# Performance work log

Measured on AMD Instinct MI355X. Metric: run time of the kernel, lower is better.

Reference implementation:

```python
import jax, jax.numpy as jnp
import numpy as np

B, C, HH, WW = 8, 640, 32, 32
NH = 8            # num heads
GROUPS = 32       # GroupNorm groups (normalization(channels))
EPS = 1e-5


def group_norm(x, w, b):
    # x: [B, C, H, W]; GroupNorm over (C/G, H, W) per group
    bb, c, hh, ww = x.shape
    xg = x.reshape(bb, GROUPS, c // GROUPS, hh, ww)
    mu = xg.mean(axis=(2, 3, 4), keepdims=True)
    var = xg.var(axis=(2, 3, 4), keepdims=True)
    xg = (xg - mu) * jax.lax.rsqrt(var + EPS)
    x = xg.reshape(bb, c, hh, ww)
    return x * w[None, :, None, None] + b[None, :, None, None]


def setup_inputs() -> dict:
    key = jax.random.key(0)
    ks = jax.random.split(key, 4)
    x = jax.random.normal(ks[0], (B, C, HH, WW), dtype=jnp.float32)
    norm_w = jnp.ones((C,), dtype=jnp.float32)
    norm_b = jnp.zeros((C,), dtype=jnp.float32)
    # 1x1 conv weights (squeezed to [out, in]); scaled for numerical sanity.
    qkv_w = jax.random.normal(ks[1], (3 * C, C), dtype=jnp.float32) / np.sqrt(C)
    qkv_b = jnp.zeros((3 * C,), dtype=jnp.float32)
    # proj_out is zero_module in the original; use random weights so the math is exercised.
    proj_w = jax.random.normal(ks[2], (C, C), dtype=jnp.float32) / np.sqrt(C)
    proj_b = jnp.zeros((C,), dtype=jnp.float32)
    return {"x": x, "norm_w": norm_w, "norm_b": norm_b,
            "qkv_w": qkv_w, "qkv_b": qkv_b, "proj_w": proj_w, "proj_b": proj_b}


def reference(x, norm_w, norm_b, qkv_w, qkv_b, proj_w, proj_b):
    b, c, hh, ww = x.shape
    T = hh * ww
    d = c // NH  # head dim
    xn = group_norm(x, norm_w, norm_b).reshape(b, c, T)          # [B,C,T]
    qkv = jnp.einsum('oc,bct->bot', qkv_w, xn) + qkv_b[None, :, None]  # [B,3C,T]
    # legacy layout: width = (three, heads, d)
    qkv = qkv.reshape(b, 3, NH, d, T)
    q, k, v = qkv[:, 0], qkv[:, 1], qkv[:, 2]                    # each [B,H,D,T]
    scale = 1.0 / jnp.sqrt(jnp.sqrt(jnp.float32(d)))
    scores = jnp.einsum('bhdt,bhds->bhts', q * scale, k * scale)  # [B,H,T,T]
    w = jax.nn.softmax(scores, axis=-1)
    a = jnp.einsum('bhts,bhds->bhdt', w, v).reshape(b, c, T)     # [B,C,T]
    h = jnp.einsum('oc,bct->bot', proj_w, a) + proj_b[None, :, None]
    return x + h.reshape(b, c, hh, ww)
```

## Files before the change

kernel.cpp:

```cpp
#include <hip/hip_runtime.h>

#define B_   8
#define C_   640
#define T_   1024
#define NH_  8
#define D_   80
#define DP_  96

typedef __attribute__((ext_vector_type(8))) short s16x8;
typedef __attribute__((ext_vector_type(4))) float f32x4;

__device__ __forceinline__ unsigned short f2b(float f) {
  unsigned u = __builtin_bit_cast(unsigned, f);
  u += 0x7FFFu + ((u >> 16) & 1u);
  return (unsigned short)(u >> 16);
}
__device__ __forceinline__ unsigned short f2bt(float f) {
  return (unsigned short)(__builtin_bit_cast(unsigned, f) >> 16);
}

__device__ __forceinline__ void gl_lds(const unsigned short* gp, unsigned short* lp) {
  __builtin_amdgcn_global_load_lds(
      (const __attribute__((address_space(1))) unsigned int*)gp,
      (__attribute__((address_space(3))) unsigned int*)lp, 16, 0, 0);
}

__global__ __launch_bounds__(256) void pre_kernel(
    const float* __restrict__ x, const float* __restrict__ w,
    const float* __restrict__ bias, unsigned short* __restrict__ xnt,
    const float* __restrict__ qw, const float* __restrict__ pw,
    unsigned short* __restrict__ oq, unsigned short* __restrict__ op) {
  const int tid = threadIdx.x;
  if (blockIdx.x >= 256) {
    const int NQ = 3 * C_ * C_ / 4, NP = C_ * C_ / 4;
    int i = (blockIdx.x - 256) * 256 + tid;
    for (; i < NQ + NP; i += 400 * 256) {
      const bool q = i < NQ;
      const float4 v = q ? ((const float4*)qw)[i] : ((const float4*)pw)[i - NQ];
      ushort4 o;
      o.x = f2b(v.x); o.y = f2b(v.y); o.z = f2b(v.z); o.w = f2b(v.w);
      if (q) ((ushort4*)oq)[i] = o; else ((ushort4*)op)[i - NQ] = o;
    }
    return;
  }
  const int b = blockIdx.x >> 5, g = blockIdx.x & 31;
  const size_t base = ((size_t)b * C_ + g * 20) * T_;
  float s = 0.f, ss = 0.f;
  for (int i = tid; i < 20 * T_; i += 256) {
    const float v = x[base + i];
    s += v; ss += v * v;
  }
  #pragma unroll
  for (int mask = 1; mask < 64; mask <<= 1) {
    s += __shfl_xor(s, mask); ss += __shfl_xor(ss, mask);
  }
  __shared__ float red[2][4];
  if ((tid & 63) == 0) { red[0][tid >> 6] = s; red[1][tid >> 6] = ss; }
  __syncthreads();
  s  = red[0][0] + red[0][1] + red[0][2] + red[0][3];
  ss = red[1][0] + red[1][1] + red[1][2] + red[1][3];
  const float mu   = s * (1.f / 20480.f);
  const float var  = ss * (1.f / 20480.f) - mu * mu;
  const float rstd = rsqrtf(var + 1e-5f);
  float ac[20], bc[20];
  #pragma unroll
  for (int c = 0; c < 20; c++) {
    const float wc = w[g * 20 + c];
    ac[c] = wc * rstd;
    bc[c] = bias[g * 20 + c] - mu * ac[c];
  }
  for (int tc = tid; tc < T_; tc += 256) {
    const size_t xoff = base + tc;
    unsigned short* dst = xnt + ((size_t)b * T_ + tc) * C_ + g * 20;
    #pragma unroll
    for (int j = 0; j < 5; j++) {
      ushort4 o;
      o.x = f2b(x[xoff + (size_t)(j * 4 + 0) * T_] * ac[j * 4 + 0] + bc[j * 4 + 0]);
      o.y = f2b(x[xoff + (size_t)(j * 4 + 1) * T_] * ac[j * 4 + 1] + bc[j * 4 + 1]);
      o.z = f2b(x[xoff + (size_t)(j * 4 + 2) * T_] * ac[j * 4 + 2] + bc[j * 4 + 2]);
      o.w = f2b(x[xoff + (size_t)(j * 4 + 3) * T_] * ac[j * 4 + 3] + bc[j * 4 + 3]);
      *(ushort4*)(dst + j * 4) = o;
    }
  }
}

template <int MODE>
__global__ __launch_bounds__(MODE == 0 ? 512 : 256, 4) void gemm_mfma(
    const unsigned short* __restrict__ Wb, const unsigned short* __restrict__ Xb,
    const float* __restrict__ bias, const float* __restrict__ resid,
    unsigned short* __restrict__ qg, unsigned short* __restrict__ kg,
    unsigned short* __restrict__ vg, float* __restrict__ outf) {
  constexpr int AUSH = MODE == 0 ? 4096 : 2048;
  constexpr int BUFU = MODE == 0 ? 12288 : 6144;
  constexpr int MF   = MODE == 0 ? 4 : 2;
  constexpr int NIT  = C_ / 32;
  __shared__ __align__(16) char smem[MODE == 0 ? 73728 : 36864];
  unsigned short* const sm = (unsigned short*)smem;
  const int tid = threadIdx.x;
  const int lane = tid & 63, wvi = tid >> 6;
  const int wm = MODE == 0 ? (wvi >> 2) : (wvi >> 1);
  const int wn = MODE == 0 ? (wvi & 3) : (wvi & 1);
  const int rl = lane & 15, gq = lane >> 4;
  const int NM = (MODE == 0) ? 15 : 10;
  const int lid = blockIdx.x + NM * (blockIdx.y + (MODE == 0 ? 4 : 8) * blockIdx.z);
  const int bz = lid & 7;
  const int mn = lid >> 3;
  const int m0 = (mn % NM) * (MODE == 0 ? 128 : 64);
  const int n0 = (mn / NM) * (MODE == 0 ? 256 : 128);
  const unsigned short* Xbb = Xb + (size_t)bz * T_ * C_;

  f32x4 acc[MF][4];
  const f32x4 zed = {0.f, 0.f, 0.f, 0.f};
  #pragma unroll
  for (int i = 0; i < MF; i++)
    #pragma unroll
    for (int j = 0; j < 4; j++) acc[i][j] = zed;

  auto STAGE = [&](int buf, int k0) {
    unsigned short* const Ab = sm + buf * BUFU;
    unsigned short* const Bb = Ab + AUSH;
    if constexpr (MODE == 0) {
      #pragma unroll
      for (int it = 0; it < 3; it++) {
        const int chunk = it * 512 + tid;
        if (chunk < 512) {
          const int row = chunk >> 2;
          const int gs = (chunk & 3) ^ ((row >> 1) & 3);
          gl_lds(Wb + (size_t)(m0 + row) * C_ + k0 + gs * 8, Ab + (tid & ~63) * 8);
        } else {
          const int c2 = chunk - 512;
          const int row = c2 >> 2;
          const int gs = (c2 & 3) ^ ((row >> 1) & 3);
          gl_lds(Xbb + (size_t)(n0 + row) * C_ + k0 + gs * 8,
                 Bb + ((it - 1) * 512 + (tid & ~63)) * 8);
        }
      }
    } else {
      #pragma unroll
      for (int it = 0; it < 3; it++) {
        const int chunk = it * 256 + tid;
        if (it == 0) {
          const int row = chunk >> 2;
          const int gs = (chunk & 3) ^ ((row >> 1) & 3);
          gl_lds(Wb + (size_t)(m0 + row) * C_ + k0 + gs * 8, Ab + (tid & ~63) * 8);
        } else {
          const int c2 = chunk - 256;
          const int row = c2 >> 2;
          const int gs = (c2 & 3) ^ ((row >> 1) & 3);
          gl_lds(Xbb + (size_t)(n0 + row) * C_ + k0 + gs * 8,
                 Bb + ((it - 1) * 256 + (tid & ~63)) * 8);
        }
      }
    }
  };

  STAGE(0, 0);
  int cur = 0;
  for (int kk = 0; kk < NIT; kk++) {
    if (kk + 1 < NIT) {
      STAGE((cur + 1) % 3, (kk + 1) * 32);
      asm volatile("s_waitcnt vmcnt(3)" ::: "memory");
    } else {
      asm volatile("s_waitcnt vmcnt(0)" ::: "memory");
    }
    __builtin_amdgcn_s_barrier();
    __builtin_amdgcn_sched_barrier(0);
    const unsigned short* As = sm + cur * BUFU;
    const unsigned short* Bs = As + AUSH;
    s16x8 af[MF], bfr[4];
    #pragma unroll
    for (int mf = 0; mf < MF; mf++) {
      const int row = wm * (MF * 16) + mf * 16 + rl;
      const int sl = gq ^ ((row >> 1) & 3);
      af[mf] = *(const s16x8*)&As[row * 32 + sl * 8];
    }
    #pragma unroll
    for (int nf = 0; nf < 4; nf++) {
      const int row = wn * 64 + nf * 16 + rl;
      const int sl = gq ^ ((row >> 1) & 3);
      bfr[nf] = *(const s16x8*)&Bs[row * 32 + sl * 8];
    }
    __builtin_amdgcn_s_setprio(1);
    #pragma unroll
    for (int mf = 0; mf < MF; mf++)
      #pragma unroll
      for (int nf = 0; nf < 4; nf++)
        acc[mf][nf] = __builtin_amdgcn_mfma_f32_16x16x32_bf16(af[mf], bfr[nf],
                                                              acc[mf][nf], 0, 0, 0);
    __builtin_amdgcn_s_setprio(0);
    cur = (cur + 1) % 3;
  }
  __syncthreads();

  if constexpr (MODE == 1) {
    #pragma unroll
    for (int mf = 0; mf < MF; mf++)
      #pragma unroll
      for (int reg = 0; reg < 4; reg++) {
        const int o = m0 + wm * 32 + mf * 16 + gq * 4 + reg;
        const float bsv = bias[o];
        #pragma unroll
        for (int nf = 0; nf < 4; nf++) {
          const int tcol = n0 + wn * 64 + nf * 16 + rl;
          const size_t idx = ((size_t)bz * C_ + o) * T_ + tcol;
          outf[idx] = acc[mf][nf][reg] + bsv + resid[idx];
        }
      }
  } else {
    const bool isV = (m0 >= 2 * C_);
    if (isV) {
      #pragma unroll
      for (int mf = 0; mf < MF; mf++)
        #pragma unroll
        for (int reg = 0; reg < 4; reg++) {
          const int o = m0 + wm * 64 + mf * 16 + gq * 4 + reg;
          const float bsv = bias[o];
          const int od = o - 2 * C_;
          const int hh = od / 80, dd = od % 80;
          #pragma unroll
          for (int nf = 0; nf < 4; nf++) {
            const int t = n0 + wn * 64 + nf * 16 + rl;
            vg[(((size_t)bz * 8 + hh) * 80 + dd) * T_ + t] = f2b(acc[mf][nf][reg] + bsv);
          }
        }
    } else {
      const int which = (m0 >= C_) ? 1 : 0;
      const float osc = which ? 1.f : (0.11180339887498948f * 1.4426950408889634f);
      const int DSTR = which ? 80 : DP_;
      unsigned short* dst0 = which ? kg : qg;
      const int m0eff = m0 - which * C_;
      unsigned short* const L = sm + (wvi & 3) * (64 * 72);
      const int phase = wvi >> 2;
      #pragma unroll
      for (int ph = 0; ph < 2; ph++) {
        if (ph == 1) __syncthreads();
        if (phase == ph) {
          #pragma unroll
          for (int mf = 0; mf < MF; mf++)
            #pragma unroll
            for (int reg = 0; reg < 4; reg++) {
              const int o = m0 + wm * 64 + mf * 16 + gq * 4 + reg;
              const float bsv = bias[o];
              #pragma unroll
              for (int nf = 0; nf < 4; nf++)
                L[(nf * 16 + rl) * 72 + mf * 16 + gq * 4 + reg] =
                    f2b((acc[mf][nf][reg] + bsv) * osc);
            }
          #pragma unroll
          for (int it = 0; it < 8; it++) {
            const int idx = it * 64 + lane;
            const int tl = idx >> 3, seg = idx & 7;
            const uint4 v = *(const uint4*)&L[tl * 72 + seg * 8];
            const int oseg = m0eff + wm * 64 + seg * 8;
            const int hh = oseg / 80, d0 = oseg % 80;
            const int t = n0 + wn * 64 + tl;
            *(uint4*)&dst0[(((size_t)bz * 8 + hh) * T_ + t) * DSTR + d0] = v;
          }
          if (which == 0) {
            const int msBase = m0eff + wm * 64;
            const int h0 = msBase / 80, h1 = (msBase + 63) / 80;
            const uint4 z4 = make_uint4(0u, 0u, 0u, 0u);
            for (int hh2 = h0; hh2 <= h1; hh2++) {
              const int t = n0 + wn * 64 + lane;
              unsigned short* pd = dst0 + (((size_t)bz * 8 + hh2) * T_ + t) * DP_ + 80;
              *(uint4*)pd = z4;
              *(uint4*)(pd + 8) = z4;
            }
          }
        }
      }
    }
  }
}

__global__ __launch_bounds__(256, 4) void flash_mfma(
    const unsigned short* __restrict__ Qg, const unsigned short* __restrict__ Kg,
    const unsigned short* __restrict__ Vg, unsigned short* __restrict__ at) {
  __shared__ __align__(16) unsigned short Kdb[2][10 * 64 * 8];
  __shared__ __align__(16) unsigned short Vs[8 * 80 * 8];
  __shared__ __align__(16) unsigned short Ps[4][16 * 72];
  const int bh = blockIdx.x, qt = blockIdx.y;
  const int b = bh >> 3, h = bh & 7;
  const int tid = threadIdx.x, lane = tid & 63, wvi = tid >> 6;
  const int rl = lane & 15, gq = lane >> 4;
  const unsigned short* Qt = Qg + ((size_t)bh * T_ + qt * 64) * DP_;
  const unsigned short* Kb = Kg + (size_t)bh * T_ * 80;
  const unsigned short* Vb = Vg + (size_t)bh * 80 * T_;

  {
    unsigned short* const qbase = (unsigned short*)Kdb;
    #pragma unroll
    for (int it = 0; it < 3; it++) {
      const int c = it * 256 + tid;
      const int row = c & 63, sl = c >> 6;
      gl_lds(Qt + (size_t)row * DP_ + sl * 8, qbase + (it * 256 + (tid & ~63)) * 8);
    }
  }
  __syncthreads();
  s16x8 qf[3];
  #pragma unroll
  for (int ks = 0; ks < 3; ks++)
    qf[ks] = *(const s16x8*)((unsigned short*)Kdb +
                             ((ks * 4 + gq) * 64 + wvi * 16 + rl) * 8);
  __syncthreads();

  auto STAGE_K = [&](int buf, int ti) {
    const int ko = ti * 64 * 80;
    #pragma unroll
    for (int it = 0; it < 3; it++) {
      if (it < 2 || tid < 128) {
        const int c = it * 256 + tid;
        const int row = c & 63, sl = c >> 6;
        gl_lds(Kb + ko + (size_t)row * 80 + sl * 8,
               Kdb[buf] + (it * 256 + (tid & ~63)) * 8);
      }
    }
  };
  auto STAGE_V = [&](int ti) {
    const int vo = ti * 64;
    #pragma unroll
    for (int it = 0; it < 3; it++) {
      if (it < 2 || tid < 128) {
        const int c = it * 256 + tid;
        const int d = c % 80, s8 = (c / 80) * 8;
        gl_lds(Vb + (size_t)d * T_ + vo + s8, Vs + (it * 256 + (tid & ~63)) * 8);
      }
    }
  };

  const f32x4 zed = {0.f, 0.f, 0.f, 0.f};
  f32x4 o_[5];
  float m_[4], l_[4];
  #pragma unroll
  for (int i = 0; i < 5; i++) o_[i] = zed;
  #pragma unroll
  for (int i = 0; i < 4; i++) { m_[i] = -1e30f; l_[i] = 0.f; }

  STAGE_K(0, 0);
  STAGE_V(0);
  __syncthreads();

  for (int ti = 0; ti < 16; ti++) {
    const int cur = ti & 1;
    if (ti > 0) STAGE_V(ti);
    if (ti + 1 < 16) STAGE_K(cur ^ 1, ti + 1);
    const unsigned short* Kc = Kdb[cur];

    f32x4 s_[4];
    #pragma unroll
    for (int nf = 0; nf < 4; nf++) s_[nf] = zed;
    __builtin_amdgcn_s_setprio(1);
    #pragma unroll
    for (int nf = 0; nf < 4; nf++)
      #pragma unroll
      for (int ks = 0; ks < 3; ks++) {
        const int sl = (ks < 2) ? (ks * 4 + gq) : (8 + (gq & 1));
        const s16x8 kf = *(const s16x8*)&Kc[(sl * 64 + nf * 16 + rl) * 8];
        s_[nf] = __builtin_amdgcn_mfma_f32_16x16x32_bf16(qf[ks], kf, s_[nf], 0, 0, 0);
      }
    __builtin_amdgcn_s_setprio(0);

    unsigned short* const Pw = Ps[wvi];
    #pragma unroll
    for (int reg = 0; reg < 4; reg++) {
      const float v0 = s_[0][reg], v1 = s_[1][reg];
      const float v2 = s_[2][reg], v3 = s_[3][reg];
      const float mold = m_[reg];
      const float lmx = fmaxf(fmaxf(v0, v1), fmaxf(v2, v3));
      float p0, p1, p2, p3;
      if (__all(lmx <= mold + 8.f)) {
        p0 = __builtin_exp2f(v0 - mold); p1 = __builtin_exp2f(v1 - mold);
        p2 = __builtin_exp2f(v2 - mold); p3 = __builtin_exp2f(v3 - mold);
        l_[reg] += p0 + p1 + p2 + p3;
      } else {
        float mx = lmx;
        mx = fmaxf(mx, __shfl_xor(mx, 1)); mx = fmaxf(mx, __shfl_xor(mx, 2));
        mx = fmaxf(mx, __shfl_xor(mx, 4)); mx = fmaxf(mx, __shfl_xor(mx, 8));
        const float nm = fmaxf(mold, mx);
        const float corr = __builtin_exp2f(mold - nm);
        p0 = __builtin_exp2f(v0 - nm); p1 = __builtin_exp2f(v1 - nm);
        p2 = __builtin_exp2f(v2 - nm); p3 = __builtin_exp2f(v3 - nm);
        l_[reg] = l_[reg] * corr + (p0 + p1 + p2 + p3);
        m_[reg] = nm;
        #pragma unroll
        for (int df = 0; df < 5; df++) o_[df][reg] *= corr;
      }
      unsigned short* const pr = Pw + (gq * 4 + reg) * 72;
      pr[rl]      = f2bt(p0);
      pr[16 + rl] = f2bt(p1);
      pr[32 + rl] = f2bt(p2);
      pr[48 + rl] = f2bt(p3);
    }
    __syncthreads();

    #pragma unroll
    for (int kc = 0; kc < 2; kc++) {
      const s16x8 pf = *(const s16x8*)&Pw[rl * 72 + kc * 32 + gq * 8];
      __builtin_amdgcn_s_setprio(1);
      #pragma unroll
      for (int df = 0; df < 5; df++) {
        const s16x8 vf = *(const s16x8*)&Vs[((kc * 4 + gq) * 80 + df * 16 + rl) * 8];
        o_[df] = __builtin_amdgcn_mfma_f32_16x16x32_bf16(pf, vf, o_[df], 0, 0, 0);
      }
      __builtin_amdgcn_s_setprio(0);
    }
    __syncthreads();
  }

  #pragma unroll
  for (int reg = 0; reg < 4; reg++) {
    float l = l_[reg];
    l += __shfl_xor(l, 1); l += __shfl_xor(l, 2);
    l += __shfl_xor(l, 4); l += __shfl_xor(l, 8);
    const float inv = 1.f / l;
    const int t = qt * 64 + wvi * 16 + gq * 4 + reg;
    #pragma unroll
    for (int df = 0; df < 5; df++)
      at[((size_t)b * T_ + t) * C_ + h * 80 + df * 16 + rl] = f2b(o_[df][reg] * inv);
  }
}

extern "C" void kernel_launch(void* const* d_in, const int* in_sizes, int n_in,
                              void* d_out, int out_size, void* d_ws, size_t ws_size,
                              hipStream_t stream) {
  const float* x      = (const float*)d_in[0];
  const float* norm_w = (const float*)d_in[1];
  const float* norm_b = (const float*)d_in[2];
  const float* qkv_w  = (const float*)d_in[3];
  const float* qkv_b  = (const float*)d_in[4];
  const float* proj_w = (const float*)d_in[5];
  const float* proj_b = (const float*)d_in[6];
  float* out = (float*)d_out;

  char* ws = (char*)d_ws;
  const size_t SEG  = (size_t)B_ * T_ * C_ * 2;
  const size_t SEGP = (size_t)B_ * NH_ * T_ * DP_ * 2;
  unsigned short* xnt = (unsigned short*)ws;
  unsigned short* Qb  = (unsigned short*)(ws + SEG);
  unsigned short* Kb2 = (unsigned short*)(ws + SEG + SEGP);
  unsigned short* Vb2 = (unsigned short*)(ws + 2 * SEG + SEGP);
  unsigned short* atb = (unsigned short*)(ws + 3 * SEG + SEGP);
  unsigned short* wq  = (unsigned short*)(ws + 4 * SEG + SEGP);
  unsigned short* wp  = (unsigned short*)(ws + 4 * SEG + SEGP + (size_t)3 * C_ * C_ * 2);

  pre_kernel<<<dim3(656), dim3(256), 0, stream>>>(x, norm_w, norm_b, xnt,
                                                  qkv_w, proj_w, wq, wp);
  gemm_mfma<0><<<dim3(15, 4, 8), dim3(512), 0, stream>>>(wq, xnt, qkv_b, nullptr,
                                                         Qb, Kb2, Vb2, nullptr);
  flash_mfma<<<dim3(64, 16), dim3(256), 0, stream>>>(Qb, Kb2, Vb2, atb);
  gemm_mfma<1><<<dim3(10, 8, 8), dim3(256), 0, stream>>>(wp, atb, proj_b, x,
                                                         nullptr, nullptr, nullptr, out);
}
```

Baseline: 135.8 us.

## Restructure flash attention to 128-query tiles with split-K waves and merge

The flash attention kernel now processes 128 queries per block with 8 waves. Each pair of waves shares a 32-query slice and splits each 64-key tile into two 32-key halves, keeping separate online-softmax state per half. The two partial results are merged through LDS at the end. This halves K/V staging traffic per query and reuses each K fragment across two query MFMAs. The cost is more registers, an extra LDS merge phase, and half as many blocks in the grid.

```diff
diff --git a/kernel.cpp b/kernel.cpp
--- a/kernel.cpp
+++ b/kernel.cpp
@@ -273,150 +273,198 @@
   }
 }
 
-__global__ __launch_bounds__(256, 4) void flash_mfma(
+__global__ __launch_bounds__(512, 4) void flash_mfma(
     const unsigned short* __restrict__ Qg, const unsigned short* __restrict__ Kg,
     const unsigned short* __restrict__ Vg, unsigned short* __restrict__ at) {
-  __shared__ __align__(16) unsigned short Kdb[2][10 * 64 * 8];
-  __shared__ __align__(16) unsigned short Vs[8 * 80 * 8];
-  __shared__ __align__(16) unsigned short Ps[4][16 * 72];
+  __shared__ __align__(16) char arena[51200];
+  unsigned short* const Kdb = (unsigned short*)arena;
+  unsigned short* const Vs  = (unsigned short*)(arena + 20480);
+  unsigned short* const Ps  = (unsigned short*)(arena + 30720);
   const int bh = blockIdx.x, qt = blockIdx.y;
   const int b = bh >> 3, h = bh & 7;
   const int tid = threadIdx.x, lane = tid & 63, wvi = tid >> 6;
   const int rl = lane & 15, gq = lane >> 4;
-  const unsigned short* Qt = Qg + ((size_t)bh * T_ + qt * 64) * DP_;
+  const int wq = wvi >> 1, wk = wvi & 1;
+  const unsigned short* Qt = Qg + ((size_t)bh * T_ + qt * 128) * DP_;
   const unsigned short* Kb = Kg + (size_t)bh * T_ * 80;
   const unsigned short* Vb = Vg + (size_t)bh * 80 * T_;
 
   {
-    unsigned short* const qbase = (unsigned short*)Kdb;
+    unsigned short* const qbase = (unsigned short*)arena;
     #pragma unroll
     for (int it = 0; it < 3; it++) {
-      const int c = it * 256 + tid;
-      const int row = c & 63, sl = c >> 6;
-      gl_lds(Qt + (size_t)row * DP_ + sl * 8, qbase + (it * 256 + (tid & ~63)) * 8);
+      const int c = it * 512 + tid;
+      const int row = c & 127, sl = c >> 7;
+      gl_lds(Qt + (size_t)row * DP_ + sl * 8, qbase + (it * 512 + (tid & ~63)) * 8);
     }
   }
   __syncthreads();
-  s16x8 qf[3];
+  s16x8 qf[2][3];
   #pragma unroll
-  for (int ks = 0; ks < 3; ks++)
-    qf[ks] = *(const s16x8*)((unsigned short*)Kdb +
-                             ((ks * 4 + gq) * 64 + wvi * 16 + rl) * 8);
+  for (int mfq = 0; mfq < 2; mfq++)
+    #pragma unroll
+    for (int ks = 0; ks < 3; ks++)
+      qf[mfq][ks] = *(const s16x8*)((unsigned short*)arena +
+                                    ((ks * 4 + gq) * 128 + wq * 32 + mfq * 16 + rl) * 8);
   __syncthreads();
 
   auto STAGE_K = [&](int buf, int ti) {
     const int ko = ti * 64 * 80;
-    #pragma unroll
-    for (int it = 0; it < 3; it++) {
-      if (it < 2 || tid < 128) {
-        const int c = it * 256 + tid;
+    unsigned short* const KL = Kdb + buf * 5120;
+    #pragma unroll
+    for (int it = 0; it < 2; it++) {
+      if (it < 1 || tid < 128) {
+        const int c = it * 512 + tid;
         const int row = c & 63, sl = c >> 6;
-        gl_lds(Kb + ko + (size_t)row * 80 + sl * 8,
-               Kdb[buf] + (it * 256 + (tid & ~63)) * 8);
+        gl_lds(Kb + ko + (size_t)row * 80 + sl * 8, KL + (it * 512 + (tid & ~63)) * 8);
       }
     }
   };
   auto STAGE_V = [&](int ti) {
     const int vo = ti * 64;
     #pragma unroll
-    for (int it = 0; it < 3; it++) {
-      if (it < 2 || tid < 128) {
-        const int c = it * 256 + tid;
+    for (int it = 0; it < 2; it++) {
+      if (it < 1 || tid < 128) {
+        const int c = it * 512 + tid;
         const int d = c % 80, s8 = (c / 80) * 8;
-        gl_lds(Vb + (size_t)d * T_ + vo + s8, Vs + (it * 256 + (tid & ~63)) * 8);
+        gl_lds(Vb + (size_t)d * T_ + vo + s8, Vs + (it * 512 + (tid & ~63)) * 8);
       }
     }
   };
 
   const f32x4 zed = {0.f, 0.f, 0.f, 0.f};
-  f32x4 o_[5];
-  float m_[4], l_[4];
+  f32x4 o_[2][5];
+  float m_[2][4], l_[2][4];
   #pragma unroll
-  for (int i = 0; i < 5; i++) o_[i] = zed;
-  #pragma unroll
-  for (int i = 0; i < 4; i++) { m_[i] = -1e30f; l_[i] = 0.f; }
+  for (int q = 0; q < 2; q++) {
+    #pragma unroll
+    for (int i = 0; i < 5; i++) o_[q][i] = zed;
+    #pragma unroll
+    for (int i = 0; i < 4; i++) { m_[q][i] = -1e30f; l_[q][i] = 0.f; }
+  }
 
   STAGE_K(0, 0);
   STAGE_V(0);
   __syncthreads();
 
+  unsigned short* const Pw = Ps + wvi * 1280;
   for (int ti = 0; ti < 16; ti++) {
     const int cur = ti & 1;
     if (ti > 0) STAGE_V(ti);
     if (ti + 1 < 16) STAGE_K(cur ^ 1, ti + 1);
-    const unsigned short* Kc = Kdb[cur];
-
-    f32x4 s_[4];
-    #pragma unroll
-    for (int nf = 0; nf < 4; nf++) s_[nf] = zed;
+    const unsigned short* Kc = Kdb + cur * 5120;
+
+    f32x4 s_[2][2];
+    #pragma unroll
+    for (int q = 0; q < 2; q++)
+      #pragma unroll
+      for (int nf = 0; nf < 2; nf++) s_[q][nf] = zed;
     __builtin_amdgcn_s_setprio(1);
     #pragma unroll
-    for (int nf = 0; nf < 4; nf++)
+    for (int nf = 0; nf < 2; nf++)
       #pragma unroll
       for (int ks = 0; ks < 3; ks++) {
         const int sl = (ks < 2) ? (ks * 4 + gq) : (8 + (gq & 1));
-        const s16x8 kf = *(const s16x8*)&Kc[(sl * 64 + nf * 16 + rl) * 8];
-        s_[nf] = __builtin_amdgcn_mfma_f32_16x16x32_bf16(qf[ks], kf, s_[nf], 0, 0, 0);
+        const s16x8 kf = *(const s16x8*)&Kc[(sl * 64 + wk * 32 + nf * 16 + rl) * 8];
+        s_[0][nf] = __builtin_amdgcn_mfma_f32_16x16x32_bf16(qf[0][ks], kf, s_[0][nf], 0, 0, 0);
+        s_[1][nf] = __builtin_amdgcn_mfma_f32_16x16x32_bf16(qf[1][ks], kf, s_[1][nf], 0, 0, 0);
       }
     __builtin_amdgcn_s_setprio(0);
 
-    unsigned short* const Pw = Ps[wvi];
-    #pragma unroll
-    for (int reg = 0; reg < 4; reg++) {
-      const float v0 = s_[0][reg], v1 = s_[1][reg];
-      const float v2 = s_[2][reg], v3 = s_[3][reg];
-      const float mold = m_[reg];
-      const float lmx = fmaxf(fmaxf(v0, v1), fmaxf(v2, v3));
-      float p0, p1, p2, p3;
-      if (__all(lmx <= mold + 8.f)) {
-        p0 = __builtin_exp2f(v0 - mold); p1 = __builtin_exp2f(v1 - mold);
-        p2 = __builtin_exp2f(v2 - mold); p3 = __builtin_exp2f(v3 - mold);
-        l_[reg] += p0 + p1 + p2 + p3;
-      } else {
-        float mx = lmx;
-        mx = fmaxf(mx, __shfl_xor(mx, 1)); mx = fmaxf(mx, __shfl_xor(mx, 2));
-        mx = fmaxf(mx, __shfl_xor(mx, 4)); mx = fmaxf(mx, __shfl_xor(mx, 8));
-        const float nm = fmaxf(mold, mx);
-        const float corr = __builtin_exp2f(mold - nm);
-        p0 = __builtin_exp2f(v0 - nm); p1 = __builtin_exp2f(v1 - nm);
-        p2 = __builtin_exp2f(v2 - nm); p3 = __builtin_exp2f(v3 - nm);
-        l_[reg] = l_[reg] * corr + (p0 + p1 + p2 + p3);
-        m_[reg] = nm;
+    #pragma unroll
+    for (int mfq = 0; mfq < 2; mfq++)
+      #pragma unroll
+      for (int reg = 0; reg < 4; reg++) {
+        const float v0 = s_[mfq][0][reg], v1 = s_[mfq][1][reg];
+        const float mold = m_[mfq][reg];
+        const float lmx = fmaxf(v0, v1);
+        float p0, p1;
+        if (__all(lmx <= mold + 8.f)) {
+          p0 = __builtin_exp2f(v0 - mold); p1 = __builtin_exp2f(v1 - mold);
+          l_[mfq][reg] += p0 + p1;
+        } else {
+          float mx = lmx;
+          mx = fmaxf(mx, __shfl_xor(mx, 1)); mx = fmaxf(mx, __shfl_xor(mx, 2));
+          mx = fmaxf(mx, __shfl_xor(mx, 4)); mx = fmaxf(mx, __shfl_xor(mx, 8));
+          const float nm = fmaxf(mold, mx);
+          const float corr = __builtin_exp2f(mold - nm);
+          p0 = __builtin_exp2f(v0 - nm); p1 = __builtin_exp2f(v1 - nm);
+          l_[mfq][reg] = l_[mfq][reg] * corr + (p0 + p1);
+          m_[mfq][reg] = nm;
+          #pragma unroll
+          for (int df = 0; df < 5; df++) o_[mfq][df][reg] *= corr;
+        }
+        unsigned short* const pr = Pw + (mfq * 16 + gq * 4 + reg) * 40;
+        pr[rl]      = f2bt(p0);
+        pr[16 + rl] = f2bt(p1);
+      }
+    __syncthreads();
+
+    s16x8 pf[2];
+    #pragma unroll
+    for (int mfq = 0; mfq < 2; mfq++)
+      pf[mfq] = *(const s16x8*)&Pw[(mfq * 16 + rl) * 40 + gq * 8];
+    __builtin_amdgcn_s_setprio(1);
+    #pragma unroll
+    for (int df = 0; df < 5; df++) {
+      const s16x8 vf = *(const s16x8*)&Vs[((wk * 4 + gq) * 80 + df * 16 + rl) * 8];
+      o_[0][df] = __builtin_amdgcn_mfma_f32_16x16x32_bf16(pf[0], vf, o_[0][df], 0, 0, 0);
+      o_[1][df] = __builtin_amdgcn_mfma_f32_16x16x32_bf16(pf[1], vf, o_[1][df], 0, 0, 0);
+    }
+    __builtin_amdgcn_s_setprio(0);
+    __syncthreads();
+  }
+
+  __syncthreads();
+  float*  const MLb = (float*)(arena + 20480);
+  f32x4*  const Ob  = (f32x4*)arena;
+  const int pid = wq * 64 + lane;
+  #pragma unroll
+  for (int mfq = 0; mfq < 2; mfq++) {
+    if (wk == 1) {
+      *(f32x4*)&MLb[pid * 8]     = *(f32x4*)&m_[mfq][0];
+      *(f32x4*)&MLb[pid * 8 + 4] = *(f32x4*)&l_[mfq][0];
+      #pragma unroll
+      for (int df = 0; df < 5; df++) Ob[df * 256 + pid] = o_[mfq][df];
+    }
+    __syncthreads();
+    if (wk == 0) {
+      const f32x4 m1 = *(const f32x4*)&MLb[pid * 8];
+      const f32x4 l1 = *(const f32x4*)&MLb[pid * 8 + 4];
+      f32x4 s0, s1;
+      #pragma unroll
+      for (int reg = 0; reg < 4; reg++) {
+        const float nm = fmaxf(m_[mfq][reg], m1[reg]);
+        s0[reg] = __builtin_exp2f(m_[mfq][reg] - nm);
+        s1[reg] = __builtin_exp2f(m1[reg] - nm);
+        l_[mfq][reg] = l_[mfq][reg] * s0[reg] + l1[reg] * s1[reg];
+      }
+      #pragma unroll
+      for (int df = 0; df < 5; df++) {
+        const f32x4 o1 = Ob[df * 256 + pid];
         #pragma unroll
-        for (int df = 0; df < 5; df++) o_[df][reg] *= corr;
-      }
-      unsigned short* const pr = Pw + (gq * 4 + reg) * 72;
-      pr[rl]      = f2bt(p0);
-      pr[16 + rl] = f2bt(p1);
-      pr[32 + rl] = f2bt(p2);
-      pr[48 + rl] = f2bt(p3);
+        for (int reg = 0; reg < 4; reg++)
+          o_[mfq][df][reg] = o_[mfq][df][reg] * s0[reg] + o1[reg] * s1[reg];
+      }
     }
     __syncthreads();
-
-    #pragma unroll
-    for (int kc = 0; kc < 2; kc++) {
-      const s16x8 pf = *(const s16x8*)&Pw[rl * 72 + kc * 32 + gq * 8];
-      __builtin_amdgcn_s_setprio(1);
-      #pragma unroll
-      for (int df = 0; df < 5; df++) {
-        const s16x8 vf = *(const s16x8*)&Vs[((kc * 4 + gq) * 80 + df * 16 + rl) * 8];
-        o_[df] = __builtin_amdgcn_mfma_f32_16x16x32_bf16(pf, vf, o_[df], 0, 0, 0);
-      }
-      __builtin_amdgcn_s_setprio(0);
-    }
-    __syncthreads();
-  }
-
-  #pragma unroll
-  for (int reg = 0; reg < 4; reg++) {
-    float l = l_[reg];
-    l += __shfl_xor(l, 1); l += __shfl_xor(l, 2);
-    l += __shfl_xor(l, 4); l += __shfl_xor(l, 8);
-    const float inv = 1.f / l;
-    const int t = qt * 64 + wvi * 16 + gq * 4 + reg;
-    #pragma unroll
-    for (int df = 0; df < 5; df++)
-      at[((size_t)b * T_ + t) * C_ + h * 80 + df * 16 + rl] = f2b(o_[df][reg] * inv);
+  }
+
+  if (wk == 0) {
+    #pragma unroll
+    for (int mfq = 0; mfq < 2; mfq++)
+      #pragma unroll
+      for (int reg = 0; reg < 4; reg++) {
+        float l = l_[mfq][reg];
+        l += __shfl_xor(l, 1); l += __shfl_xor(l, 2);
+        l += __shfl_xor(l, 4); l += __shfl_xor(l, 8);
+        const float inv = 1.f / l;
+        const int t = qt * 128 + wq * 32 + mfq * 16 + gq * 4 + reg;
+        #pragma unroll
+        for (int df = 0; df < 5; df++)
+          at[((size_t)b * T_ + t) * C_ + h * 80 + df * 16 + rl] =
+              f2b(o_[mfq][df][reg] * inv);
+      }
   }
 }
 
@@ -447,7 +495,7 @@
                                                   qkv_w, proj_w, wq, wp);
   gemm_mfma<0><<<dim3(15, 4, 8), dim3(512), 0, stream>>>(wq, xnt, qkv_b, nullptr,
                                                          Qb, Kb2, Vb2, nullptr);
-  flash_mfma<<<dim3(64, 16), dim3(256), 0, stream>>>(Qb, Kb2, Vb2, atb);
+  flash_mfma<<<dim3(64, 8), dim3(512), 0, stream>>>(Qb, Kb2, Vb2, atb);
   gemm_mfma<1><<<dim3(10, 8, 8), dim3(256), 0, stream>>>(wp, atb, proj_b, x,
                                                          nullptr, nullptr, nullptr, out);
 }
```

Result: slower. 179.7 us (+32.3%).
